# Kernel optimization log

Measured on AMD Instinct MI355X. Metric: run time of the kernel, lower is better.

The kernel has to match this reference:

```python
import jax, jax.numpy as jnp
import numpy as np

HID = 64
L = 5
N_NODES = 50000
N_EDGES = 1600000
N_GRAPHS = 4
EPS = 1e-5


def _ln(h, g, b):
    m = jnp.mean(h, axis=-1, keepdims=True)
    v = jnp.mean((h - m) ** 2, axis=-1, keepdims=True)
    return (h - m) * jax.lax.rsqrt(v + EPS) * g + b


def _lin_init(key, fan_in, fan_out):
    return jax.random.normal(key, (fan_in, fan_out), jnp.float32) / np.sqrt(fan_in)


def setup_inputs() -> dict:
    key = jax.random.key(0)
    ks = jax.random.split(key, 24)
    inp = {}
    inp['x'] = jax.random.normal(ks[0], (N_NODES, 8), jnp.float32)
    inp['edge_index'] = jax.random.randint(ks[1], (2, N_EDGES), 0, N_NODES)
    inp['edge_attr'] = jax.random.normal(ks[2], (N_EDGES, 5), jnp.float32)
    inp['batch'] = jnp.sort(jax.random.randint(ks[3], (N_NODES,), 0, N_GRAPHS))
    inp['case_params'] = jax.random.normal(ks[4], (N_GRAPHS, 4), jnp.float32)
    inp['bc_params'] = jax.random.normal(ks[5], (N_GRAPHS, 4), jnp.float32)
    # encoder
    inp['enc_W1'] = _lin_init(ks[6], 16, HID); inp['enc_b1'] = jnp.zeros((HID,))
    inp['enc_W2'] = _lin_init(ks[7], HID, HID); inp['enc_b2'] = jnp.zeros((HID,))
    inp['enc_g'] = jnp.ones((HID,)); inp['enc_be'] = jnp.zeros((HID,))
    # processor (stacked over L layers)
    ek = jax.random.split(ks[8], L); nk = jax.random.split(ks[9], L)
    ek2 = jax.random.split(ks[10], L); nk2 = jax.random.split(ks[11], L)
    inp['eW1'] = jnp.stack([_lin_init(ek[i], 2 * HID + 5, HID) for i in range(L)])
    inp['eb1'] = jnp.zeros((L, HID))
    inp['eW2'] = jnp.stack([_lin_init(ek2[i], HID, HID) for i in range(L)])
    inp['eb2'] = jnp.zeros((L, HID))
    inp['eg'] = jnp.ones((L, HID)); inp['ebe'] = jnp.zeros((L, HID))
    inp['nW1'] = jnp.stack([_lin_init(nk[i], 2 * HID, HID) for i in range(L)])
    inp['nb1'] = jnp.zeros((L, HID))
    inp['nW2'] = jnp.stack([_lin_init(nk2[i], HID, HID) for i in range(L)])
    inp['nb2'] = jnp.zeros((L, HID))
    inp['ng'] = jnp.ones((L, HID)); inp['nbe'] = jnp.zeros((L, HID))
    # decoders
    inp['dlW1'] = _lin_init(ks[12], HID, HID); inp['dlb1'] = jnp.zeros((HID,))
    inp['dlW2'] = _lin_init(ks[13], HID, 6); inp['dlb2'] = jnp.zeros((6,))
    inp['dgW1'] = _lin_init(ks[14], HID, HID // 2); inp['dgb1'] = jnp.zeros((HID // 2,))
    inp['dgW2'] = _lin_init(ks[15], HID // 2, 4); inp['dgb2'] = jnp.zeros((4,))
    return inp


def reference(x, edge_index, edge_attr, batch, case_params, bc_params,
              enc_W1, enc_b1, enc_W2, enc_b2, enc_g, enc_be,
              eW1, eb1, eW2, eb2, eg, ebe,
              nW1, nb1, nW2, nb2, ng, nbe,
              dlW1, dlb1, dlW2, dlb2, dgW1, dgb1, dgW2, dgb2):
    n_nodes = x.shape[0]
    n_graphs = case_params.shape[0]
    silu = jax.nn.silu
    # input concat: node feats + per-graph globals gathered by batch index
    gv = jnp.concatenate([case_params, bc_params], axis=1)  # [B, 8]
    h = jnp.concatenate([x, gv[batch]], axis=1)             # [N, 16]
    # encoder
    h = _ln(silu(h @ enc_W1 + enc_b1) @ enc_W2 + enc_b2, enc_g, enc_be)
    src, dst = edge_index[0], edge_index[1]  # PyG: x_j = src, x_i = dst
    n_layers = eW1.shape[0]
    for l in range(n_layers):
        xi = h[dst]  # [E, H] target
        xj = h[src]  # [E, H] source
        m = jnp.concatenate([xi, xj, edge_attr], axis=1)  # [E, 2H+5]
        m = _ln(silu(m @ eW1[l] + eb1[l]) @ eW2[l] + eb2[l], eg[l], ebe[l])
        agg = jax.ops.segment_sum(m, dst, num_segments=n_nodes)  # scatter-add
        t = jnp.concatenate([h, agg], axis=1)  # [N, 2H]
        h = h + _ln(silu(t @ nW1[l] + nb1[l]) @ nW2[l] + nb2[l], ng[l], nbe[l])
    out_local = silu(h @ dlW1 + dlb1) @ dlW2 + dlb2  # [N, 6]
    cnt = jax.ops.segment_sum(jnp.ones((n_nodes,), h.dtype), batch, num_segments=n_graphs)
    pooled = jax.ops.segment_sum(h, batch, num_segments=n_graphs) / jnp.maximum(cnt, 1.0)[:, None]
    out_global = silu(pooled @ dgW1 + dgb1) @ dgW2 + dgb2  # [B, 4]
    return (out_local, out_global)
```

## Files before the change

### kernel.cpp

```cpp
#include <hip/hip_runtime.h>
#include <cmath>

constexpr int NN = 50000;
constexpr int NE = 1600000;
constexpr int H  = 64;
constexpr int NL = 5;
constexpr int NG = 4;
constexpr int EIN = 2 * H + 5;
constexpr int NIN = 2 * H;

typedef short bf16x8 __attribute__((ext_vector_type(8)));
typedef float f32x4  __attribute__((ext_vector_type(4)));

__device__ __forceinline__ float silu_f(float x) {
    return x / (1.0f + __expf(-x));
}

__device__ __forceinline__ unsigned int f2bf(float f) {
    unsigned int u = __float_as_uint(f);
    u += 0x7fffu + ((u >> 16) & 1u);
    return u >> 16;
}
__device__ __forceinline__ unsigned int pack_bf16x2(float x, float y) {
    return f2bf(x) | (f2bf(y) << 16);
}

template <int CTRL>
__device__ __forceinline__ int dpp_i(int old, int v) {
    return __builtin_amdgcn_update_dpp(old, v, CTRL, 0xF, 0xF, false);
}

__global__ __launch_bounds__(256) void degree_kernel(
    const int* __restrict__ ei, int* __restrict__ deg)
{
    int e = blockIdx.x * 256 + threadIdx.x;
    if (e < NE) atomicAdd(&deg[ei[NE + e]], 1);
}

__global__ __launch_bounds__(1024) void scan1_kernel(
    const int* __restrict__ deg, int* __restrict__ off, int* __restrict__ bsum)
{
    __shared__ int sh[1024];
    const int tid = threadIdx.x;
    int i = blockIdx.x * 1024 + tid;
    int v = (i < NN) ? deg[i] : 0;
    sh[tid] = v;
    __syncthreads();
    for (int d = 1; d < 1024; d <<= 1) {
        int t = (tid >= d) ? sh[tid - d] : 0;
        __syncthreads();
        sh[tid] += t;
        __syncthreads();
    }
    if (i < NN) off[i] = sh[tid] - v;
    if (tid == 1023) bsum[blockIdx.x] = sh[1023];
}

__global__ __launch_bounds__(64) void scan2_kernel(
    const int* __restrict__ bsum, int* __restrict__ bbase, int nb)
{
    int lane = threadIdx.x;
    int v = (lane < nb) ? bsum[lane] : 0;
    int orig = v;
    for (int d = 1; d < 64; d <<= 1) {
        int t = __shfl_up(v, d);
        if (lane >= d) v += t;
    }
    bbase[lane] = v - orig;
}

__global__ __launch_bounds__(1024) void scan3_kernel(
    int* __restrict__ off, const int* __restrict__ bbase,
    int* __restrict__ cursor)
{
    int i = blockIdx.x * 1024 + threadIdx.x;
    if (i < NN) {
        int o = off[i] + bbase[blockIdx.x];
        off[i] = o;
        cursor[i] = o;
        if (i == NN - 1) off[NN] = NE;
    }
}

__global__ __launch_bounds__(256) void scatter_kernel(
    const int* __restrict__ ei, int* __restrict__ cursor,
    int* __restrict__ sidx, int* __restrict__ sdst, int* __restrict__ ssrc)
{
    int e = blockIdx.x * 256 + threadIdx.x;
    if (e < NE) {
        int d = ei[NE + e];
        int p = atomicAdd(&cursor[d], 1);
        sidx[p] = e;
        sdst[p] = d;
        ssrc[p] = ei[e];
    }
}

__global__ __launch_bounds__(256) void ea_pack_kernel(
    const float* __restrict__ ea, const int* __restrict__ sidx,
    uint4* __restrict__ ea_pk)
{
    int p = blockIdx.x * 256 + threadIdx.x;
    if (p < NE) {
        const float* s = ea + (size_t)sidx[p] * 5;
        uint4 v;
        v.x = pack_bf16x2(s[0], s[1]);
        v.y = pack_bf16x2(s[2], s[3]);
        v.z = pack_bf16x2(s[4], 0.0f);
        v.w = 0u;
        ea_pk[p] = v;
    }
}

__global__ __launch_bounds__(256) void pack_weights_kernel(
    const float* __restrict__ eW1, const float* __restrict__ eW2,
    const float* __restrict__ nW1, const float* __restrict__ nW2,
    const float* __restrict__ dlW1, const float* __restrict__ dlW2,
    short* __restrict__ eW1pk, short* __restrict__ eW2pk,
    short* __restrict__ nW1pk, short* __restrict__ nW2pk,
    short* __restrict__ dlW1pk, short* __restrict__ dlW2pk)
{
    int l = blockIdx.y;
    int t = blockIdx.x * 256 + threadIdx.x;
    if (t < 10240) {
        int j = t & 7, lane = (t >> 3) & 63, mt = (t >> 9) & 3, ks = t >> 11;
        int k  = ks * 32 + (lane >> 4) * 8 + j;
        int ch = mt * 16 + (lane & 15);
        float v = (k < EIN) ? eW1[(size_t)l * EIN * H + k * H + ch] : 0.0f;
        eW1pk[(size_t)l * 10240 + t] = (short)f2bf(v);
    } else if (t < 14336) {
        int t2 = t - 10240;
        int j = t2 & 7, lane = (t2 >> 3) & 63, mt = (t2 >> 9) & 3, ks = t2 >> 11;
        int k = ks * 32 + (lane >> 4) * 8 + j;
        int ch = mt * 16 + (lane & 15);
        eW2pk[(size_t)l * 4096 + t2] = (short)f2bf(eW2[(size_t)l * H * H + k * H + ch]);
    } else if (t < 22528) {
        int t3 = t - 14336;
        int j = t3 & 7, lane = (t3 >> 3) & 63, mt = (t3 >> 9) & 3, ks = t3 >> 11;
        int k = ks * 32 + (lane >> 4) * 8 + j;
        int ch = mt * 16 + (lane & 15);
        nW1pk[(size_t)l * 8192 + t3] = (short)f2bf(nW1[(size_t)l * NIN * H + k * H + ch]);
    } else if (t < 26624) {
        int t4 = t - 22528;
        int j = t4 & 7, lane = (t4 >> 3) & 63, mt = (t4 >> 9) & 3, ks = t4 >> 11;
        int k = ks * 32 + (lane >> 4) * 8 + j;
        int ch = mt * 16 + (lane & 15);
        nW2pk[(size_t)l * 4096 + t4] = (short)f2bf(nW2[(size_t)l * H * H + k * H + ch]);
    } else if (t < 30720) {
        if (l == 0) {
            int t5 = t - 26624;
            int j = t5 & 7, lane = (t5 >> 3) & 63, mt = (t5 >> 9) & 3, ks = t5 >> 11;
            int k = ks * 32 + (lane >> 4) * 8 + j;
            int ch = mt * 16 + (lane & 15);
            dlW1pk[t5] = (short)f2bf(dlW1[k * H + ch]);
        }
    } else if (t < 31744) {
        if (l == 0) {
            int t6 = t - 30720;
            int j = t6 & 7, lane = (t6 >> 3) & 63, ks = t6 >> 9;
            int k = ks * 32 + (lane >> 4) * 8 + j;
            int m = lane & 15;
            float v = (m < 6) ? dlW2[k * 6 + m] : 0.0f;
            dlW2pk[t6] = (short)f2bf(v);
        }
    }
}

__global__ __launch_bounds__(256) void encoder_kernel(
    const float* __restrict__ x, const int* __restrict__ batch,
    const float* __restrict__ case_p, const float* __restrict__ bc_p,
    const float* __restrict__ W1, const float* __restrict__ b1,
    const float* __restrict__ W2, const float* __restrict__ b2,
    const float* __restrict__ g, const float* __restrict__ be,
    float* __restrict__ h, unsigned int* __restrict__ h2)
{
    __shared__ float in_sh[64 * 17];
    __shared__ float m1_sh[64 * 65];
    __shared__ float red_sh[2 * 4 * 64];
    const int lane = threadIdx.x & 63;
    const int w    = threadIdx.x >> 6;
    const int wb   = __builtin_amdgcn_readfirstlane(w * 16);
    const int n0   = blockIdx.x * 64;

    for (int i = 0; i < 16; ++i) {
        int slot = w * 16 + i;
        int n = n0 + slot;
        if (n < NN && lane < 16) {
            float v;
            if (lane < 8) v = x[n * 8 + lane];
            else {
                int b = batch[n];
                v = (lane < 12) ? case_p[b * 4 + (lane - 8)]
                                : bc_p[b * 4 + (lane - 12)];
            }
            in_sh[slot * 17 + lane] = v;
        }
    }
    __syncthreads();

    float acc[16];
#pragma unroll
    for (int c = 0; c < 16; ++c) acc[c] = b1[wb + c];
    for (int k = 0; k < 16; ++k) {
        float a = in_sh[lane * 17 + k];
        const float4* wr = (const float4*)(W1 + k * 64 + wb);
        float4 w0 = wr[0], w1 = wr[1], w2 = wr[2], w3 = wr[3];
        acc[0]  = fmaf(a, w0.x, acc[0]);  acc[1]  = fmaf(a, w0.y, acc[1]);
        acc[2]  = fmaf(a, w0.z, acc[2]);  acc[3]  = fmaf(a, w0.w, acc[3]);
        acc[4]  = fmaf(a, w1.x, acc[4]);  acc[5]  = fmaf(a, w1.y, acc[5]);
        acc[6]  = fmaf(a, w1.z, acc[6]);  acc[7]  = fmaf(a, w1.w, acc[7]);
        acc[8]  = fmaf(a, w2.x, acc[8]);  acc[9]  = fmaf(a, w2.y, acc[9]);
        acc[10] = fmaf(a, w2.z, acc[10]); acc[11] = fmaf(a, w2.w, acc[11]);
        acc[12] = fmaf(a, w3.x, acc[12]); acc[13] = fmaf(a, w3.y, acc[13]);
        acc[14] = fmaf(a, w3.z, acc[14]); acc[15] = fmaf(a, w3.w, acc[15]);
    }
#pragma unroll
    for (int c = 0; c < 16; ++c) m1_sh[lane * 65 + wb + c] = silu_f(acc[c]);
    __syncthreads();

    float acc2[16];
#pragma unroll
    for (int c = 0; c < 16; ++c) acc2[c] = b2[wb + c];
    for (int k = 0; k < 64; ++k) {
        float a = m1_sh[lane * 65 + k];
        const float4* wr = (const float4*)(W2 + k * 64 + wb);
        float4 w0 = wr[0], w1 = wr[1], w2 = wr[2], w3 = wr[3];
        acc2[0]  = fmaf(a, w0.x, acc2[0]);  acc2[1]  = fmaf(a, w0.y, acc2[1]);
        acc2[2]  = fmaf(a, w0.z, acc2[2]);  acc2[3]  = fmaf(a, w0.w, acc2[3]);
        acc2[4]  = fmaf(a, w1.x, acc2[4]);  acc2[5]  = fmaf(a, w1.y, acc2[5]);
        acc2[6]  = fmaf(a, w1.z, acc2[6]);  acc2[7]  = fmaf(a, w1.w, acc2[7]);
        acc2[8]  = fmaf(a, w2.x, acc2[8]);  acc2[9]  = fmaf(a, w2.y, acc2[9]);
        acc2[10] = fmaf(a, w2.z, acc2[10]); acc2[11] = fmaf(a, w2.w, acc2[11]);
        acc2[12] = fmaf(a, w3.x, acc2[12]); acc2[13] = fmaf(a, w3.y, acc2[13]);
        acc2[14] = fmaf(a, w3.z, acc2[14]); acc2[15] = fmaf(a, w3.w, acc2[15]);
    }

    float s1 = 0.f, s2 = 0.f;
#pragma unroll
    for (int c = 0; c < 16; ++c) { s1 += acc2[c]; s2 += acc2[c] * acc2[c]; }
    red_sh[w * 64 + lane] = s1;
    red_sh[256 + w * 64 + lane] = s2;
    __syncthreads();
    float t1 = 0.f, t2 = 0.f;
#pragma unroll
    for (int j = 0; j < 4; ++j) {
        t1 += red_sh[j * 64 + lane];
        t2 += red_sh[256 + j * 64 + lane];
    }
    float mean = t1 * (1.0f / 64.0f);
    float var  = t2 * (1.0f / 64.0f) - mean * mean;
    float rstd = rsqrtf(var + 1e-5f);

    int n = n0 + lane;
    if (n < NN) {
        float vals[16];
#pragma unroll
        for (int c = 0; c < 16; ++c) {
            int ch = wb + c;
            vals[c] = (acc2[c] - mean) * rstd * g[ch] + be[ch];
            h[n * 64 + ch] = vals[c];
        }
        uint4 p0, p1;
        p0.x = pack_bf16x2(vals[0], vals[1]);   p0.y = pack_bf16x2(vals[2], vals[3]);
        p0.z = pack_bf16x2(vals[4], vals[5]);   p0.w = pack_bf16x2(vals[6], vals[7]);
        p1.x = pack_bf16x2(vals[8], vals[9]);   p1.y = pack_bf16x2(vals[10], vals[11]);
        p1.z = pack_bf16x2(vals[12], vals[13]); p1.w = pack_bf16x2(vals[14], vals[15]);
        *(uint4*)(h2 + (size_t)n * 32 + w * 8)     = p0;
        *(uint4*)(h2 + (size_t)n * 32 + w * 8 + 4) = p1;
    }
}

__global__ __launch_bounds__(256, 7) void edge_kernel(
    const unsigned int* __restrict__ h2,
    const int* __restrict__ sdst, const int* __restrict__ ssrc,
    const uint4* __restrict__ ea_pk,
    const short* __restrict__ W1pk, const float* __restrict__ b1,
    const short* __restrict__ W2pk, const float* __restrict__ b2,
    const float* __restrict__ g, const float* __restrict__ be,
    float* __restrict__ agg)
{
    __shared__ unsigned int lds[4 * 1088];
    const int lane = threadIdx.x & 63;
    const int w    = threadIdx.x >> 6;
    const int quad = lane >> 4;
    const int l15  = lane & 15;
    const int tile = (blockIdx.x & 7) * 3125 + (blockIdx.x >> 3);
    const int e0   = tile * 64 + w * 16;
    unsigned int* B1  = lds + w * 1088;
    unsigned int* MID = B1;

    union { uint4 u; bf16x8 b; } eacv;
    eacv.u = ea_pk[e0 + l15];
    const bf16x8 zfrag = {0, 0, 0, 0, 0, 0, 0, 0};
    const bf16x8 ks4frag = (quad == 0) ? eacv.b : zfrag;

#pragma unroll
    for (int i = 0; i < 4; ++i) {
        int hr   = i * 8 + (lane >> 3);
        int p    = e0 + (hr >> 1);
        int node = (hr & 1) ? ssrc[p] : sdst[p];
        int w4   = (lane & 7) * 4;
        uint4 v = *(const uint4*)(h2 + (size_t)node * 32 + w4);
        *(uint4*)(B1 + (hr >> 1) * 68 + (hr & 1) * 32 + w4) = v;
    }

    f32x4 acc1[4] = {{0,0,0,0},{0,0,0,0},{0,0,0,0},{0,0,0,0}};
    const unsigned int* brow = B1 + l15 * 68;
    for (int ks = 0; ks < 4; ++ks) {
        bf16x8 bfrag = *(const bf16x8*)(brow + ks * 16 + quad * 4);
        const short* apk = W1pk + (size_t)(ks * 4) * 512 + lane * 8;
#pragma unroll
        for (int mt = 0; mt < 4; ++mt) {
            bf16x8 afrag = *(const bf16x8*)(apk + mt * 512);
            acc1[mt] = __builtin_amdgcn_mfma_f32_16x16x32_bf16(
                afrag, bfrag, acc1[mt], 0, 0, 0);
        }
    }
    {
        const short* apk = W1pk + (size_t)(4 * 4) * 512 + lane * 8;
#pragma unroll
        for (int mt = 0; mt < 4; ++mt) {
            bf16x8 afrag = *(const bf16x8*)(apk + mt * 512);
            acc1[mt] = __builtin_amdgcn_mfma_f32_16x16x32_bf16(
                afrag, ks4frag, acc1[mt], 0, 0, 0);
        }
    }
#pragma unroll
    for (int mt = 0; mt < 4; ++mt) {
        int ch0 = mt * 16 + quad * 4;
        float v0 = silu_f(acc1[mt][0] + b1[ch0 + 0]);
        float v1 = silu_f(acc1[mt][1] + b1[ch0 + 1]);
        float v2 = silu_f(acc1[mt][2] + b1[ch0 + 2]);
        float v3 = silu_f(acc1[mt][3] + b1[ch0 + 3]);
        uint2 pk;
        pk.x = pack_bf16x2(v0, v1);
        pk.y = pack_bf16x2(v2, v3);
        *(uint2*)(MID + l15 * 36 + mt * 8 + quad * 2) = pk;
    }

    f32x4 acc2[4] = {{0,0,0,0},{0,0,0,0},{0,0,0,0},{0,0,0,0}};
    const unsigned int* mrow = MID + l15 * 36;
    for (int ks = 0; ks < 2; ++ks) {
        bf16x8 bfrag = *(const bf16x8*)(mrow + ks * 16 + quad * 4);
        const short* apk = W2pk + (size_t)(ks * 4) * 512 + lane * 8;
#pragma unroll
        for (int mt = 0; mt < 4; ++mt) {
            bf16x8 afrag = *(const bf16x8*)(apk + mt * 512);
            acc2[mt] = __builtin_amdgcn_mfma_f32_16x16x32_bf16(
                afrag, bfrag, acc2[mt], 0, 0, 0);
        }
    }

    float vals[16];
    float s1 = 0.f, s2 = 0.f;
#pragma unroll
    for (int mt = 0; mt < 4; ++mt) {
#pragma unroll
        for (int r = 0; r < 4; ++r) {
            int ch = mt * 16 + quad * 4 + r;
            float vv = acc2[mt][r] + b2[ch];
            vals[mt * 4 + r] = vv;
            s1 += vv; s2 += vv * vv;
        }
    }
    s1 += __shfl_xor(s1, 16); s1 += __shfl_xor(s1, 32);
    s2 += __shfl_xor(s2, 16); s2 += __shfl_xor(s2, 32);
    float mean = s1 * (1.0f / 64.0f);
    float var  = s2 * (1.0f / 64.0f) - mean * mean;
    float rstd = rsqrtf(var + 1e-5f);
#pragma unroll
    for (int mt = 0; mt < 4; ++mt) {
#pragma unroll
        for (int r = 0; r < 4; ++r) {
            int ch = mt * 16 + quad * 4 + r;
            vals[mt * 4 + r] = (vals[mt * 4 + r] - mean) * rstd * g[ch] + be[ch];
        }
    }

    int d_l = sdst[e0 + l15];
#define SEG_STEP(CTRL)                                                        \
    {                                                                         \
        int d_up = dpp_i<CTRL>(-1, d_l);                                      \
        float msk = (d_up == d_l) ? 1.0f : 0.0f;                              \
        _Pragma("unroll")                                                     \
        for (int c = 0; c < 16; ++c) {                                        \
            float vu = __int_as_float(dpp_i<CTRL>(0, __float_as_int(vals[c])));\
            vals[c] = fmaf(vu, msk, vals[c]);                                 \
        }                                                                     \
    }
    SEG_STEP(0x111)
    SEG_STEP(0x112)
    SEG_STEP(0x114)
    SEG_STEP(0x118)
#undef SEG_STEP
    int d_next = dpp_i<0x101>(-1, d_l);
    bool last = (d_next != d_l);
    if (last) {
#pragma unroll
        for (int mt = 0; mt < 4; ++mt) {
#pragma unroll
            for (int r = 0; r < 4; ++r) {
                int ch = mt * 16 + quad * 4 + r;
                atomicAdd(&agg[(size_t)d_l * 64 + ch], vals[mt * 4 + r]);
            }
        }
    }
}

__global__ __launch_bounds__(256, 6) void node_kernel(
    float* __restrict__ h, unsigned int* __restrict__ h2,
    const float* __restrict__ agg,
    const short* __restrict__ W1pk, const float* __restrict__ b1,
    const short* __restrict__ W2pk, const float* __restrict__ b2,
    const float* __restrict__ g, const float* __restrict__ be)
{
    __shared__ unsigned int lds[4 * 1088];
    const int lane = threadIdx.x & 63;
    const int w    = threadIdx.x >> 6;
    const int quad = lane >> 4;
    const int l15  = lane & 15;
    const int n0   = blockIdx.x * 64 + w * 16;
    unsigned int* B1  = lds + w * 1088;
    unsigned int* MID = B1;

#pragma unroll
    for (int i = 0; i < 2; ++i) {
        int row = i * 8 + (lane >> 3);
        int n = n0 + row; if (n >= NN) n = NN - 1;
        int w4 = (lane & 7) * 4;
        uint4 v = *(const uint4*)(h2 + (size_t)n * 32 + w4);
        *(uint4*)(B1 + row * 68 + w4) = v;
    }
#pragma unroll
    for (int i = 0; i < 4; ++i) {
        int row = i * 4 + (lane >> 4);
        int n = n0 + row; if (n >= NN) n = NN - 1;
        int f4 = lane & 15;
        float4 v = *(const float4*)(agg + (size_t)n * 64 + f4 * 4);
        uint2 pk;
        pk.x = pack_bf16x2(v.x, v.y);
        pk.y = pack_bf16x2(v.z, v.w);
        *(uint2*)(B1 + row * 68 + 32 + f4 * 2) = pk;
    }

    f32x4 acc1[4] = {{0,0,0,0},{0,0,0,0},{0,0,0,0},{0,0,0,0}};
    const unsigned int* brow = B1 + l15 * 68;
    for (int ks = 0; ks < 4; ++ks) {
        bf16x8 bfrag = *(const bf16x8*)(brow + ks * 16 + quad * 4);
        const short* apk = W1pk + (size_t)(ks * 4) * 512 + lane * 8;
#pragma unroll
        for (int mt = 0; mt < 4; ++mt) {
            bf16x8 afrag = *(const bf16x8*)(apk + mt * 512);
            acc1[mt] = __builtin_amdgcn_mfma_f32_16x16x32_bf16(
                afrag, bfrag, acc1[mt], 0, 0, 0);
        }
    }
#pragma unroll
    for (int mt = 0; mt < 4; ++mt) {
        int ch0 = mt * 16 + quad * 4;
        float v0 = silu_f(acc1[mt][0] + b1[ch0 + 0]);
        float v1 = silu_f(acc1[mt][1] + b1[ch0 + 1]);
        float v2 = silu_f(acc1[mt][2] + b1[ch0 + 2]);
        float v3 = silu_f(acc1[mt][3] + b1[ch0 + 3]);
        uint2 pk;
        pk.x = pack_bf16x2(v0, v1);
        pk.y = pack_bf16x2(v2, v3);
        *(uint2*)(MID + l15 * 36 + mt * 8 + quad * 2) = pk;
    }

    f32x4 acc2[4] = {{0,0,0,0},{0,0,0,0},{0,0,0,0},{0,0,0,0}};
    const unsigned int* mrow = MID + l15 * 36;
    for (int ks = 0; ks < 2; ++ks) {
        bf16x8 bfrag = *(const bf16x8*)(mrow + ks * 16 + quad * 4);
        const short* apk = W2pk + (size_t)(ks * 4) * 512 + lane * 8;
#pragma unroll
        for (int mt = 0; mt < 4; ++mt) {
            bf16x8 afrag = *(const bf16x8*)(apk + mt * 512);
            acc2[mt] = __builtin_amdgcn_mfma_f32_16x16x32_bf16(
                afrag, bfrag, acc2[mt], 0, 0, 0);
        }
    }

    float vals[16];
    float s1 = 0.f, s2 = 0.f;
#pragma unroll
    for (int mt = 0; mt < 4; ++mt) {
#pragma unroll
        for (int r = 0; r < 4; ++r) {
            int ch = mt * 16 + quad * 4 + r;
            float vv = acc2[mt][r] + b2[ch];
            vals[mt * 4 + r] = vv;
            s1 += vv; s2 += vv * vv;
        }
    }
    s1 += __shfl_xor(s1, 16); s1 += __shfl_xor(s1, 32);
    s2 += __shfl_xor(s2, 16); s2 += __shfl_xor(s2, 32);
    float mean = s1 * (1.0f / 64.0f);
    float var  = s2 * (1.0f / 64.0f) - mean * mean;
    float rstd = rsqrtf(var + 1e-5f);

    int n = n0 + l15;
    if (n < NN) {
#pragma unroll
        for (int mt = 0; mt < 4; ++mt) {
            int ch0 = mt * 16 + quad * 4;
            float4 hv = *(const float4*)(h + (size_t)n * 64 + ch0);
            float o0 = hv.x + (vals[mt*4+0] - mean) * rstd * g[ch0+0] + be[ch0+0];
            float o1 = hv.y + (vals[mt*4+1] - mean) * rstd * g[ch0+1] + be[ch0+1];
            float o2 = hv.z + (vals[mt*4+2] - mean) * rstd * g[ch0+2] + be[ch0+2];
            float o3 = hv.w + (vals[mt*4+3] - mean) * rstd * g[ch0+3] + be[ch0+3];
            float4 st = {o0, o1, o2, o3};
            *(float4*)(h + (size_t)n * 64 + ch0) = st;
            uint2 pk;
            pk.x = pack_bf16x2(o0, o1);
            pk.y = pack_bf16x2(o2, o3);
            *(uint2*)(h2 + (size_t)n * 32 + mt * 8 + quad * 2) = pk;
        }
    }
}

__global__ __launch_bounds__(256, 7) void dec_local_kernel(
    const unsigned int* __restrict__ h2,
    const short* __restrict__ W1pk, const float* __restrict__ b1,
    const short* __restrict__ W2pk, const float* __restrict__ b2,
    float* __restrict__ out)
{
    __shared__ unsigned int lds[4 * 576];
    const int lane = threadIdx.x & 63;
    const int w    = threadIdx.x >> 6;
    const int quad = lane >> 4;
    const int l15  = lane & 15;
    const int n0   = blockIdx.x * 64 + w * 16;
    unsigned int* B1  = lds + w * 576;
    unsigned int* MID = B1;

#pragma unroll
    for (int i = 0; i < 2; ++i) {
        int row = i * 8 + (lane >> 3);
        int n = n0 + row; if (n >= NN) n = NN - 1;
        int w4 = (lane & 7) * 4;
        uint4 v = *(const uint4*)(h2 + (size_t)n * 32 + w4);
        *(uint4*)(B1 + row * 36 + w4) = v;
    }

    f32x4 acc1[4] = {{0,0,0,0},{0,0,0,0},{0,0,0,0},{0,0,0,0}};
    const unsigned int* brow = B1 + l15 * 36;
    for (int ks = 0; ks < 2; ++ks) {
        bf16x8 bfrag = *(const bf16x8*)(brow + ks * 16 + quad * 4);
        const short* apk = W1pk + (size_t)(ks * 4) * 512 + lane * 8;
#pragma unroll
        for (int mt = 0; mt < 4; ++mt) {
            bf16x8 afrag = *(const bf16x8*)(apk + mt * 512);
            acc1[mt] = __builtin_amdgcn_mfma_f32_16x16x32_bf16(
                afrag, bfrag, acc1[mt], 0, 0, 0);
        }
    }
#pragma unroll
    for (int mt = 0; mt < 4; ++mt) {
        int ch0 = mt * 16 + quad * 4;
        float v0 = silu_f(acc1[mt][0] + b1[ch0 + 0]);
        float v1 = silu_f(acc1[mt][1] + b1[ch0 + 1]);
        float v2 = silu_f(acc1[mt][2] + b1[ch0 + 2]);
        float v3 = silu_f(acc1[mt][3] + b1[ch0 + 3]);
        uint2 pk;
        pk.x = pack_bf16x2(v0, v1);
        pk.y = pack_bf16x2(v2, v3);
        *(uint2*)(MID + l15 * 36 + mt * 8 + quad * 2) = pk;
    }

    f32x4 acc2 = {0, 0, 0, 0};
    const unsigned int* mrow = MID + l15 * 36;
    for (int ks = 0; ks < 2; ++ks) {
        bf16x8 bfrag = *(const bf16x8*)(mrow + ks * 16 + quad * 4);
        bf16x8 afrag = *(const bf16x8*)(W2pk + (size_t)ks * 512 + lane * 8);
        acc2 = __builtin_amdgcn_mfma_f32_16x16x32_bf16(afrag, bfrag, acc2, 0, 0, 0);
    }

    int n = n0 + l15;
    if (n < NN && quad < 2) {
#pragma unroll
        for (int r = 0; r < 4; ++r) {
            int ch = quad * 4 + r;
            if (ch < 6) out[(size_t)n * 6 + ch] = acc2[r] + b2[ch];
        }
    }
}

__global__ __launch_bounds__(256) void pool_kernel(
    const float* __restrict__ h, const int* __restrict__ batch,
    float* __restrict__ pooled, float* __restrict__ cnt)
{
    const int c   = threadIdx.x & 63;
    const int rep = blockIdx.x * 4 + (threadIdx.x >> 6);
    float acc[NG] = {0.f, 0.f, 0.f, 0.f};
    float cl[NG]  = {0.f, 0.f, 0.f, 0.f};
    for (int n = rep; n < NN; n += 1024) {
        int b = batch[n];
        float v = h[n * 64 + c];
#pragma unroll
        for (int gph = 0; gph < NG; ++gph) {
            if (b == gph) { acc[gph] += v; cl[gph] += 1.0f; }
        }
    }
#pragma unroll
    for (int gph = 0; gph < NG; ++gph) {
        atomicAdd(&pooled[gph * 64 + c], acc[gph]);
        if (c == 0) atomicAdd(&cnt[gph], cl[gph]);
    }
}

__global__ __launch_bounds__(256) void dec_global_kernel(
    const float* __restrict__ pooled, const float* __restrict__ cnt,
    const float* __restrict__ W1, const float* __restrict__ b1,
    const float* __restrict__ W2, const float* __restrict__ b2,
    float* __restrict__ out)
{
    __shared__ float mid_sh[4][32];
    const int lane = threadIdx.x & 63;
    const int gph  = threadIdx.x >> 6;
    float inv = 1.0f / fmaxf(cnt[gph], 1.0f);
    if (lane < 32) {
        float a = b1[lane];
        for (int k = 0; k < 64; ++k)
            a = fmaf(pooled[gph * 64 + k] * inv, W1[k * 32 + lane], a);
        mid_sh[gph][lane] = silu_f(a);
    }
    __syncthreads();
    if (lane < 4) {
        float o = b2[lane];
        for (int k = 0; k < 32; ++k)
            o = fmaf(mid_sh[gph][k], W2[k * 4 + lane], o);
        out[gph * 4 + lane] = o;
    }
}

extern "C" void kernel_launch(void* const* d_in, const int* in_sizes, int n_in,
                              void* d_out, int out_size, void* d_ws, size_t ws_size,
                              hipStream_t stream)
{
    const float* x      = (const float*)d_in[0];
    const int*   ei     = (const int*)  d_in[1];
    const float* ea     = (const float*)d_in[2];
    const int*   batch  = (const int*)  d_in[3];
    const float* case_p = (const float*)d_in[4];
    const float* bc_p   = (const float*)d_in[5];
    const float* enc_W1 = (const float*)d_in[6];
    const float* enc_b1 = (const float*)d_in[7];
    const float* enc_W2 = (const float*)d_in[8];
    const float* enc_b2 = (const float*)d_in[9];
    const float* enc_g  = (const float*)d_in[10];
    const float* enc_be = (const float*)d_in[11];
    const float* eW1    = (const float*)d_in[12];
    const float* eb1    = (const float*)d_in[13];
    const float* eW2    = (const float*)d_in[14];
    const float* eb2    = (const float*)d_in[15];
    const float* eg     = (const float*)d_in[16];
    const float* ebe    = (const float*)d_in[17];
    const float* nW1    = (const float*)d_in[18];
    const float* nb1    = (const float*)d_in[19];
    const float* nW2    = (const float*)d_in[20];
    const float* nb2    = (const float*)d_in[21];
    const float* ng     = (const float*)d_in[22];
    const float* nbe    = (const float*)d_in[23];
    const float* dlW1   = (const float*)d_in[24];
    const float* dlb1   = (const float*)d_in[25];
    const float* dlW2   = (const float*)d_in[26];
    const float* dlb2   = (const float*)d_in[27];
    const float* dgW1   = (const float*)d_in[28];
    const float* dgb1   = (const float*)d_in[29];
    const float* dgW2   = (const float*)d_in[30];
    const float* dgb2   = (const float*)d_in[31];

    float* out = (float*)d_out;

    char* ws = (char*)d_ws;
    size_t off_b = 0;
    auto alloc = [&](size_t bytes) {
        void* p = ws + off_b;
        off_b = (off_b + bytes + 255) & ~(size_t)255;
        return p;
    };
    const size_t hBytes = (size_t)NN * H * sizeof(float);
    float*        h      = (float*)alloc(hBytes);
    float*        agg    = (float*)alloc(hBytes);
    unsigned int* h2     = (unsigned int*)alloc((size_t)NN * 32 * 4);
    float*        pooled = (float*)alloc(256 * sizeof(float));
    float*        cnt    = (float*)alloc(4 * sizeof(float));
    int*          deg    = (int*)alloc((NN + 1) * sizeof(int));
    int*          offs   = (int*)alloc((NN + 1) * sizeof(int));
    int*          cursor = (int*)alloc((NN + 1) * sizeof(int));
    int*          bsum   = (int*)alloc(64 * sizeof(int));
    int*          bbase  = (int*)alloc(64 * sizeof(int));
    int*          sidx   = (int*)alloc((size_t)NE * sizeof(int));
    int*          sdst   = (int*)alloc((size_t)NE * sizeof(int));
    int*          ssrc   = (int*)alloc((size_t)NE * sizeof(int));
    uint4*        ea_pk  = (uint4*)alloc((size_t)NE * sizeof(uint4));
    short*        eW1pk  = (short*)alloc((size_t)NL * 10240 * sizeof(short));
    short*        eW2pk  = (short*)alloc((size_t)NL * 4096 * sizeof(short));
    short*        nW1pk  = (short*)alloc((size_t)NL * 8192 * sizeof(short));
    short*        nW2pk  = (short*)alloc((size_t)NL * 4096 * sizeof(short));
    short*        dlW1pk = (short*)alloc(4096 * sizeof(short));
    short*        dlW2pk = (short*)alloc(1024 * sizeof(short));

    hipMemsetAsync(pooled, 0, (256 + 4 + 64) * sizeof(float), stream);
    hipMemsetAsync(deg, 0, (NN + 1) * sizeof(int), stream);

    const int NB = (NN + 1023) / 1024;
    degree_kernel<<<(NE + 255) / 256, 256, 0, stream>>>(ei, deg);
    scan1_kernel<<<NB, 1024, 0, stream>>>(deg, offs, bsum);
    scan2_kernel<<<1, 64, 0, stream>>>(bsum, bbase, NB);
    scan3_kernel<<<NB, 1024, 0, stream>>>(offs, bbase, cursor);
    scatter_kernel<<<(NE + 255) / 256, 256, 0, stream>>>(ei, cursor, sidx, sdst, ssrc);
    ea_pack_kernel<<<(NE + 255) / 256, 256, 0, stream>>>(ea, sidx, ea_pk);
    pack_weights_kernel<<<dim3(124, NL), 256, 0, stream>>>(
        eW1, eW2, nW1, nW2, dlW1, dlW2,
        eW1pk, eW2pk, nW1pk, nW2pk, dlW1pk, dlW2pk);

    const int nodeBlocks = (NN + 63) / 64;
    encoder_kernel<<<nodeBlocks, 256, 0, stream>>>(
        x, batch, case_p, bc_p, enc_W1, enc_b1, enc_W2, enc_b2, enc_g, enc_be,
        h, h2);

    for (int l = 0; l < NL; ++l) {
        hipMemsetAsync(agg, 0, hBytes, stream);
        edge_kernel<<<NE / 64, 256, 0, stream>>>(
            h2, sdst, ssrc, ea_pk,
            eW1pk + (size_t)l * 10240, eb1 + l * H,
            eW2pk + (size_t)l * 4096,  eb2 + l * H,
            eg + l * H, ebe + l * H, agg);
        node_kernel<<<nodeBlocks, 256, 0, stream>>>(
            h, h2, agg,
            nW1pk + (size_t)l * 8192, nb1 + l * H,
            nW2pk + (size_t)l * 4096, nb2 + l * H,
            ng + l * H, nbe + l * H);
    }

    dec_local_kernel<<<nodeBlocks, 256, 0, stream>>>(
        h2, dlW1pk, dlb1, dlW2pk, dlb2, out);
    pool_kernel<<<256, 256, 0, stream>>>(h, batch, pooled, cnt);
    dec_global_kernel<<<1, 256, 0, stream>>>(pooled, cnt, dgW1, dgb1, dgW2, dgb2,
                                             out + (size_t)NN * 6);
}
```

Baseline: 1.577 ms.

## Load MFMA B-fragments directly from global memory and use hardware bf16 pack

```diff
diff --git a/kernel.cpp b/kernel.cpp
--- a/kernel.cpp
+++ b/kernel.cpp
@@ -22,7 +22,9 @@
     return u >> 16;
 }
 __device__ __forceinline__ unsigned int pack_bf16x2(float x, float y) {
-    return f2bf(x) | (f2bf(y) << 16);
+    unsigned int r;
+    asm("v_cvt_pk_bf16_f32 %0, %1, %2" : "=v"(r) : "v"(x), "v"(y));
+    return r;
 }
 
 template <int CTRL>
@@ -279,52 +281,49 @@
     const float* __restrict__ g, const float* __restrict__ be,
     float* __restrict__ agg)
 {
-    __shared__ unsigned int lds[4 * 1088];
+    __shared__ unsigned int lds[4 * 576];
     const int lane = threadIdx.x & 63;
     const int w    = threadIdx.x >> 6;
     const int quad = lane >> 4;
     const int l15  = lane & 15;
     const int tile = (blockIdx.x & 7) * 3125 + (blockIdx.x >> 3);
     const int e0   = tile * 64 + w * 16;
-    unsigned int* B1  = lds + w * 1088;
-    unsigned int* MID = B1;
+    unsigned int* MID = lds + w * 576;
+
+    const int d_l = sdst[e0 + l15];
+    const int s_l = ssrc[e0 + l15];
 
     union { uint4 u; bf16x8 b; } eacv;
     eacv.u = ea_pk[e0 + l15];
     const bf16x8 zfrag = {0, 0, 0, 0, 0, 0, 0, 0};
     const bf16x8 ks4frag = (quad == 0) ? eacv.b : zfrag;
 
-#pragma unroll
-    for (int i = 0; i < 4; ++i) {
-        int hr   = i * 8 + (lane >> 3);
-        int p    = e0 + (hr >> 1);
-        int node = (hr & 1) ? ssrc[p] : sdst[p];
-        int w4   = (lane & 7) * 4;
-        uint4 v = *(const uint4*)(h2 + (size_t)node * 32 + w4);
-        *(uint4*)(B1 + (hr >> 1) * 68 + (hr & 1) * 32 + w4) = v;
-    }
+    const unsigned int* drow = h2 + (size_t)d_l * 32 + quad * 4;
+    const unsigned int* srow = h2 + (size_t)s_l * 32 + quad * 4;
+    union { uint4 u; bf16x8 b; } bfA, bfB, bfC, bfD;
+    bfA.u = *(const uint4*)(drow);
+    bfB.u = *(const uint4*)(drow + 16);
+    bfC.u = *(const uint4*)(srow);
+    bfD.u = *(const uint4*)(srow + 16);
 
     f32x4 acc1[4] = {{0,0,0,0},{0,0,0,0},{0,0,0,0},{0,0,0,0}};
-    const unsigned int* brow = B1 + l15 * 68;
-    for (int ks = 0; ks < 4; ++ks) {
-        bf16x8 bfrag = *(const bf16x8*)(brow + ks * 16 + quad * 4);
-        const short* apk = W1pk + (size_t)(ks * 4) * 512 + lane * 8;
-#pragma unroll
-        for (int mt = 0; mt < 4; ++mt) {
-            bf16x8 afrag = *(const bf16x8*)(apk + mt * 512);
-            acc1[mt] = __builtin_amdgcn_mfma_f32_16x16x32_bf16(
-                afrag, bfrag, acc1[mt], 0, 0, 0);
-        }
-    }
-    {
-        const short* apk = W1pk + (size_t)(4 * 4) * 512 + lane * 8;
-#pragma unroll
-        for (int mt = 0; mt < 4; ++mt) {
-            bf16x8 afrag = *(const bf16x8*)(apk + mt * 512);
-            acc1[mt] = __builtin_amdgcn_mfma_f32_16x16x32_bf16(
-                afrag, ks4frag, acc1[mt], 0, 0, 0);
-        }
-    }
+#define G1_STEP(KS, BFRAG)                                                    \
+    {                                                                         \
+        const short* apk = W1pk + (size_t)((KS) * 4) * 512 + lane * 8;        \
+        _Pragma("unroll")                                                     \
+        for (int mt = 0; mt < 4; ++mt) {                                      \
+            bf16x8 afrag = *(const bf16x8*)(apk + mt * 512);                  \
+            acc1[mt] = __builtin_amdgcn_mfma_f32_16x16x32_bf16(               \
+                afrag, BFRAG, acc1[mt], 0, 0, 0);                             \
+        }                                                                     \
+    }
+    G1_STEP(0, bfA.b)
+    G1_STEP(1, bfB.b)
+    G1_STEP(2, bfC.b)
+    G1_STEP(3, bfD.b)
+    G1_STEP(4, ks4frag)
+#undef G1_STEP
+
 #pragma unroll
     for (int mt = 0; mt < 4; ++mt) {
         int ch0 = mt * 16 + quad * 4;
@@ -377,7 +376,6 @@
         }
     }
 
-    int d_l = sdst[e0 + l15];
 #define SEG_STEP(CTRL)                                                        \
     {                                                                         \
         int d_up = dpp_i<CTRL>(-1, d_l);                                      \
@@ -414,47 +412,48 @@
     const short* __restrict__ W2pk, const float* __restrict__ b2,
     const float* __restrict__ g, const float* __restrict__ be)
 {
-    __shared__ unsigned int lds[4 * 1088];
+    __shared__ unsigned int lds[4 * 576];
     const int lane = threadIdx.x & 63;
     const int w    = threadIdx.x >> 6;
     const int quad = lane >> 4;
     const int l15  = lane & 15;
     const int n0   = blockIdx.x * 64 + w * 16;
-    unsigned int* B1  = lds + w * 1088;
-    unsigned int* MID = B1;
-
-#pragma unroll
-    for (int i = 0; i < 2; ++i) {
-        int row = i * 8 + (lane >> 3);
-        int n = n0 + row; if (n >= NN) n = NN - 1;
-        int w4 = (lane & 7) * 4;
-        uint4 v = *(const uint4*)(h2 + (size_t)n * 32 + w4);
-        *(uint4*)(B1 + row * 68 + w4) = v;
-    }
-#pragma unroll
-    for (int i = 0; i < 4; ++i) {
-        int row = i * 4 + (lane >> 4);
-        int n = n0 + row; if (n >= NN) n = NN - 1;
-        int f4 = lane & 15;
-        float4 v = *(const float4*)(agg + (size_t)n * 64 + f4 * 4);
-        uint2 pk;
-        pk.x = pack_bf16x2(v.x, v.y);
-        pk.y = pack_bf16x2(v.z, v.w);
-        *(uint2*)(B1 + row * 68 + 32 + f4 * 2) = pk;
-    }
+    unsigned int* MID = lds + w * 576;
+
+    int n_l = n0 + l15; if (n_l >= NN) n_l = NN - 1;
+
+    const unsigned int* nrow = h2 + (size_t)n_l * 32 + quad * 4;
+    union { uint4 u; bf16x8 b; } bfA, bfB;
+    bfA.u = *(const uint4*)(nrow);
+    bfB.u = *(const uint4*)(nrow + 16);
+    const float* ap = agg + (size_t)n_l * 64 + quad * 8;
+    float4 a0 = *(const float4*)(ap);
+    float4 a1 = *(const float4*)(ap + 4);
+    float4 a2 = *(const float4*)(ap + 32);
+    float4 a3 = *(const float4*)(ap + 36);
+    union { unsigned int u[4]; bf16x8 b; } bfC, bfD;
+    bfC.u[0] = pack_bf16x2(a0.x, a0.y); bfC.u[1] = pack_bf16x2(a0.z, a0.w);
+    bfC.u[2] = pack_bf16x2(a1.x, a1.y); bfC.u[3] = pack_bf16x2(a1.z, a1.w);
+    bfD.u[0] = pack_bf16x2(a2.x, a2.y); bfD.u[1] = pack_bf16x2(a2.z, a2.w);
+    bfD.u[2] = pack_bf16x2(a3.x, a3.y); bfD.u[3] = pack_bf16x2(a3.z, a3.w);
 
     f32x4 acc1[4] = {{0,0,0,0},{0,0,0,0},{0,0,0,0},{0,0,0,0}};
-    const unsigned int* brow = B1 + l15 * 68;
-    for (int ks = 0; ks < 4; ++ks) {
-        bf16x8 bfrag = *(const bf16x8*)(brow + ks * 16 + quad * 4);
-        const short* apk = W1pk + (size_t)(ks * 4) * 512 + lane * 8;
-#pragma unroll
-        for (int mt = 0; mt < 4; ++mt) {
-            bf16x8 afrag = *(const bf16x8*)(apk + mt * 512);
-            acc1[mt] = __builtin_amdgcn_mfma_f32_16x16x32_bf16(
-                afrag, bfrag, acc1[mt], 0, 0, 0);
-        }
-    }
+#define G1_STEP(KS, BFRAG)                                                    \
+    {                                                                         \
+        const short* apk = W1pk + (size_t)((KS) * 4) * 512 + lane * 8;        \
+        _Pragma("unroll")                                                     \
+        for (int mt = 0; mt < 4; ++mt) {                                      \
+            bf16x8 afrag = *(const bf16x8*)(apk + mt * 512);                  \
+            acc1[mt] = __builtin_amdgcn_mfma_f32_16x16x32_bf16(               \
+                afrag, BFRAG, acc1[mt], 0, 0, 0);                             \
+        }                                                                     \
+    }
+    G1_STEP(0, bfA.b)
+    G1_STEP(1, bfB.b)
+    G1_STEP(2, bfC.b)
+    G1_STEP(3, bfD.b)
+#undef G1_STEP
+
 #pragma unroll
     for (int mt = 0; mt < 4; ++mt) {
         int ch0 = mt * 16 + quad * 4;
@@ -531,30 +530,29 @@
     const int quad = lane >> 4;
     const int l15  = lane & 15;
     const int n0   = blockIdx.x * 64 + w * 16;
-    unsigned int* B1  = lds + w * 576;
-    unsigned int* MID = B1;
-
-#pragma unroll
-    for (int i = 0; i < 2; ++i) {
-        int row = i * 8 + (lane >> 3);
-        int n = n0 + row; if (n >= NN) n = NN - 1;
-        int w4 = (lane & 7) * 4;
-        uint4 v = *(const uint4*)(h2 + (size_t)n * 32 + w4);
-        *(uint4*)(B1 + row * 36 + w4) = v;
-    }
+    unsigned int* MID = lds + w * 576;
+
+    int n_l = n0 + l15; if (n_l >= NN) n_l = NN - 1;
+    const unsigned int* nrow = h2 + (size_t)n_l * 32 + quad * 4;
+    union { uint4 u; bf16x8 b; } bfA, bfB;
+    bfA.u = *(const uint4*)(nrow);
+    bfB.u = *(const uint4*)(nrow + 16);
 
     f32x4 acc1[4] = {{0,0,0,0},{0,0,0,0},{0,0,0,0},{0,0,0,0}};
-    const unsigned int* brow = B1 + l15 * 36;
-    for (int ks = 0; ks < 2; ++ks) {
-        bf16x8 bfrag = *(const bf16x8*)(brow + ks * 16 + quad * 4);
-        const short* apk = W1pk + (size_t)(ks * 4) * 512 + lane * 8;
-#pragma unroll
-        for (int mt = 0; mt < 4; ++mt) {
-            bf16x8 afrag = *(const bf16x8*)(apk + mt * 512);
-            acc1[mt] = __builtin_amdgcn_mfma_f32_16x16x32_bf16(
-                afrag, bfrag, acc1[mt], 0, 0, 0);
-        }
-    }
+#define G1_STEP(KS, BFRAG)                                                    \
+    {                                                                         \
+        const short* apk = W1pk + (size_t)((KS) * 4) * 512 + lane * 8;        \
+        _Pragma("unroll")                                                     \
+        for (int mt = 0; mt < 4; ++mt) {                                      \
+            bf16x8 afrag = *(const bf16x8*)(apk + mt * 512);                  \
+            acc1[mt] = __builtin_amdgcn_mfma_f32_16x16x32_bf16(               \
+                afrag, BFRAG, acc1[mt], 0, 0, 0);                             \
+        }                                                                     \
+    }
+    G1_STEP(0, bfA.b)
+    G1_STEP(1, bfB.b)
+#undef G1_STEP
+
 #pragma unroll
     for (int mt = 0; mt < 4; ++mt) {
         int ch0 = mt * 16 + quad * 4;
```

New measurement: 1.590 ms. Within noise of the previous version (+0.8%).
